# Optimization experiments

Hardware: AMD Instinct MI355X
Metric: run time of the kernel (lower is better)

## Reference

```python
import jax, jax.numpy as jnp
import numpy as np

B, S, HID = 1, 2048, 3072
NH, NKV, HD = 24, 8, 128
ROT = 96
OP = NH * HD + 2 * NKV * HD
MASK_VALUE = -jnp.finfo(jnp.float32).max


def setup_inputs() -> dict:
    key = jax.random.key(0)
    k1, k2, k3, k4, k5 = jax.random.split(key, 5)
    hidden_states = jax.random.normal(k1, (B, S, HID), dtype=jnp.float32)
    # rotary embeddings: use actual cos/sin of rope angles for realism
    inv_freq = 1.0 / (10000.0 ** (jnp.arange(0, ROT, 2, dtype=jnp.float32) / ROT))
    t = jnp.arange(S, dtype=jnp.float32)
    freqs = jnp.outer(t, inv_freq)  # [S, ROT/2]
    emb = jnp.concatenate([freqs, freqs], axis=-1)  # [S, ROT]
    cos = jnp.broadcast_to(jnp.cos(emb)[None], (B, S, ROT))
    sin = jnp.broadcast_to(jnp.sin(emb)[None], (B, S, ROT))
    attention_mask = jnp.ones((B, S), dtype=bool)
    w_qkv = jax.random.normal(k2, (OP, HID), dtype=jnp.float32) * (HID ** -0.5)
    w_o = jax.random.normal(k3, (HID, HID), dtype=jnp.float32) * (HID ** -0.5)
    return {"hidden_states": hidden_states, "cos": cos, "sin": sin,
            "attention_mask": attention_mask, "w_qkv": w_qkv, "w_o": w_o}


def rotate_half(x):
    x1, x2 = jnp.split(x, 2, axis=-1)
    return jnp.concatenate([-x2, x1], axis=-1)


def apply_rope(q, k, cos, sin):
    # cos/sin: [B, S, ROT] -> [B, 1, S, ROT]
    cos = cos[:, None]
    sin = sin[:, None]
    rd = cos.shape[-1]
    q_rot, q_pass = q[..., :rd], q[..., rd:]
    k_rot, k_pass = k[..., :rd], k[..., rd:]
    q = jnp.concatenate([q_rot * cos + rotate_half(q_rot) * sin, q_pass], axis=-1)
    k = jnp.concatenate([k_rot * cos + rotate_half(k_rot) * sin, k_pass], axis=-1)
    return q, k


def reference(hidden_states, cos, sin, attention_mask, w_qkv, w_o):
    b, n, _ = hidden_states.shape
    qkv = hidden_states @ w_qkv.T  # [B, S, OP]
    q, k, v = jnp.split(qkv, [NH * HD, NH * HD + NKV * HD], axis=-1)
    # b n (h d) -> b h n d
    q = q.reshape(b, n, NH, HD).transpose(0, 2, 1, 3)
    k = k.reshape(b, n, NKV, HD).transpose(0, 2, 1, 3)
    v = v.reshape(b, n, NKV, HD).transpose(0, 2, 1, 3)
    q, k = apply_rope(q, k, cos, sin)
    q = q * (HD ** -0.5)
    n_rep = NH // NKV
    if n_rep > 1:
        k = jnp.repeat(k, n_rep, axis=1)
        v = jnp.repeat(v, n_rep, axis=1)
    sim = jnp.einsum('bhid,bhjd->bhij', q, k)
    causal = jnp.triu(jnp.ones((n, n), dtype=bool), k=1)
    sim = jnp.where(causal, MASK_VALUE, sim)
    sim = jnp.where(~attention_mask[:, None, None, :], MASK_VALUE, sim)
    attn = jax.nn.softmax(sim.astype(jnp.float32), axis=-1).astype(v.dtype)
    out = jnp.einsum('bhij,bhjd->bhid', attn, v)
    out = out.transpose(0, 2, 1, 3).reshape(b, n, NH * HD)  # b h n d -> b n (h d)
    return out @ w_o.T
```

## Files before the change

### kernel.cpp

```cpp
#include <hip/hip_runtime.h>

typedef unsigned short u16;
typedef unsigned int u32;
typedef __bf16 bf16x8 __attribute__((ext_vector_type(8)));
typedef float f32x4 __attribute__((ext_vector_type(4)));

#define S_LEN 2048
#define HIDDEN 3072
#define NHEADS 24
#define NKVH 8
#define HDIM 128
#define QKVW 5120
#define QKLD 4096
#define PSTR 80

__device__ __forceinline__ u16 f2bf(float f) {
  u32 u = __float_as_uint(f);
  u32 r = (u + 0x7fffu + ((u >> 16) & 1u)) >> 16;
  return (u16)r;
}
__device__ __forceinline__ float bf2f(u16 h) { return __uint_as_float(((u32)h) << 16); }

__device__ __forceinline__ void gload_lds16(const void* g, void* l) {
  __builtin_amdgcn_global_load_lds((const __attribute__((address_space(1))) void*)g,
                                   (__attribute__((address_space(3))) void*)l, 16, 0, 0);
}

__global__ void cast4(const float4* __restrict__ in, uint2* __restrict__ out, int n4) {
  int i = blockIdx.x * blockDim.x + threadIdx.x;
  if (i >= n4) return;
  float4 f = in[i];
  uint2 o;
  o.x = ((u32)f2bf(f.y) << 16) | f2bf(f.x);
  o.y = ((u32)f2bf(f.w) << 16) | f2bf(f.z);
  out[i] = o;
}

__global__ __launch_bounds__(512, 2) void gemm256(const u16* __restrict__ A,
                                                  const u16* __restrict__ B,
                                                  u16* __restrict__ Cb,
                                                  u16* __restrict__ vtg) {
  __shared__ u16 lds[5][13312];
  const int tid = threadIdx.x;
  const int w = tid >> 6, lane = tid & 63;
  const int wm = w & 3, wn = w >> 2;
  const int l15 = lane & 15, qd = lane >> 4;
  const int K = 3072;
  const int m0 = ((int)blockIdx.x & 7) * 256;
  const int n0 = ((int)blockIdx.x >> 3) * 160;

  size_t offA[2], offB[2];
  int ldsA[2], ldsB[2];
#pragma unroll
  for (int it = 0; it < 2; ++it) {
    int CH = w * 128 + it * 64 + lane;
    int rp = CH >> 3, sl = CH & 7;
    int lin = sl ^ (rp & 7);
    int r = (rp << 1) | (lin >> 2), q = lin & 3;
    offA[it] = (size_t)(m0 + r) * K + q * 8;
    ldsA[it] = (w * 128 + it * 64) * 8;
  }
#pragma unroll
  for (int it = 0; it < 2; ++it) {
    int CH = it * 512 + w * 64 + lane;
    int rp = CH >> 3, sl = CH & 7;
    int lin = sl ^ (rp & 7);
    int r = (rp << 1) | (lin >> 2), q = lin & 3;
    offB[it] = (size_t)(n0 + r) * K + q * 8;
    ldsB[it] = 8192 + (it * 512 + w * 64) * 8;
  }

  int chA[4], chB[5];
#pragma unroll
  for (int i = 0; i < 4; ++i) {
    int r = wm * 64 + i * 16 + l15;
    chA[i] = ((r >> 1) * 8 + ((((r & 1) << 2) | qd) ^ ((r >> 1) & 7))) * 8;
  }
#pragma unroll
  for (int j = 0; j < 5; ++j) {
    int r = wn * 80 + j * 16 + l15;
    chB[j] = 8192 + ((r >> 1) * 8 + ((((r & 1) << 2) | qd) ^ ((r >> 1) & 7))) * 8;
  }

  f32x4 acc[4][5] = {};

  auto stage = [&](int s, int k0) {
    gload_lds16(A + offA[0] + k0, &lds[s][ldsA[0]]);
    gload_lds16(A + offA[1] + k0, &lds[s][ldsA[1]]);
    gload_lds16(B + offB[0] + k0, &lds[s][ldsB[0]]);
    if (w < 2) gload_lds16(B + offB[1] + k0, &lds[s][ldsB[1]]);
  };
  auto rdf = [&](int s, bf16x8 (&Af)[4], bf16x8 (&Bf)[5]) {
#pragma unroll
    for (int i = 0; i < 4; ++i) Af[i] = *(const bf16x8*)&lds[s][chA[i]];
#pragma unroll
    for (int j = 0; j < 5; ++j) Bf[j] = *(const bf16x8*)&lds[s][chB[j]];
  };
  auto mm = [&](bf16x8 (&Af)[4], bf16x8 (&Bf)[5]) {
    __builtin_amdgcn_sched_barrier(0);
    __builtin_amdgcn_s_setprio(1);
#pragma unroll
    for (int i = 0; i < 4; ++i)
#pragma unroll
      for (int j = 0; j < 5; ++j)
        acc[i][j] = __builtin_amdgcn_mfma_f32_16x16x32_bf16(Af[i], Bf[j], acc[i][j], 0, 0, 0);
    __builtin_amdgcn_s_setprio(0);
  };

  stage(0, 0);
  stage(1, 32);
  stage(2, 64);
  stage(3, 96);
  if (w < 2) asm volatile("s_waitcnt vmcnt(8)" ::: "memory");
  else       asm volatile("s_waitcnt vmcnt(6)" ::: "memory");
  __builtin_amdgcn_s_barrier();

  bf16x8 A0[4], B0[5], A1[4], B1[5];
  rdf(0, A0, B0);

  int sp = 4, sc = 1;
  for (int t = 0; t < 92; t += 2) {
    stage(sp, (t + 4) * 32); sp = (sp == 4) ? 0 : sp + 1;
    rdf(sc, A1, B1);         sc = (sc == 4) ? 0 : sc + 1;
    mm(A0, B0);
    if (w < 2) asm volatile("s_waitcnt vmcnt(8)" ::: "memory");
    else       asm volatile("s_waitcnt vmcnt(6)" ::: "memory");
    __builtin_amdgcn_s_barrier();
    stage(sp, (t + 5) * 32); sp = (sp == 4) ? 0 : sp + 1;
    rdf(sc, A0, B0);         sc = (sc == 4) ? 0 : sc + 1;
    mm(A1, B1);
    if (w < 2) asm volatile("s_waitcnt vmcnt(8)" ::: "memory");
    else       asm volatile("s_waitcnt vmcnt(6)" ::: "memory");
    __builtin_amdgcn_s_barrier();
  }
  rdf(3, A1, B1);
  mm(A0, B0);
  if (w < 2) asm volatile("s_waitcnt vmcnt(4)" ::: "memory");
  else       asm volatile("s_waitcnt vmcnt(3)" ::: "memory");
  __builtin_amdgcn_s_barrier();
  rdf(4, A0, B0);
  mm(A1, B1);
  asm volatile("s_waitcnt vmcnt(0)" ::: "memory");
  __builtin_amdgcn_s_barrier();
  rdf(0, A1, B1);
  mm(A0, B0);
  mm(A1, B1);

#pragma unroll
  for (int j = 0; j < 5; ++j) {
    const int nf = n0 + wn * 80 + j * 16;
    if (nf >= 4096) {
#pragma unroll
      for (int i = 0; i < 4; ++i) {
        int nv = nf - 4096 + l15;
        int m = m0 + wm * 64 + i * 16 + qd * 4;
        uint2 p;
        p.x = ((u32)f2bf(acc[i][j][1]) << 16) | f2bf(acc[i][j][0]);
        p.y = ((u32)f2bf(acc[i][j][3]) << 16) | f2bf(acc[i][j][2]);
        *(uint2*)&vtg[(size_t)nv * S_LEN + m] = p;
      }
    } else {
#pragma unroll
      for (int i = 0; i < 4; ++i)
#pragma unroll
        for (int r = 0; r < 4; ++r) {
          int m = m0 + wm * 64 + i * 16 + qd * 4 + r;
          Cb[(size_t)m * QKLD + nf + l15] = f2bf(acc[i][j][r]);
        }
    }
  }
}

__global__ __launch_bounds__(512, 2) void gemm2k(const u16* __restrict__ A,
                                                 const u16* __restrict__ B,
                                                 float* __restrict__ C) {
  __shared__ u16 lds[5][10240];
  const int tid = threadIdx.x;
  const int w = tid >> 6, lane = tid & 63;
  const int wm = w & 1, wn = w >> 1;
  const int l15 = lane & 15, qd = lane >> 4;
  const int K = 3072;
  const int xcd = (int)blockIdx.x & 7, idx = (int)blockIdx.x >> 3;
  const int m0 = ((xcd & 1) * 8 + (idx & 7)) * 128;
  const int n0 = ((xcd >> 1) * 4 + (idx >> 3)) * 192;

  size_t offA, offB[2];
  int ldsAo, ldsB[2];
  {
    int CH = w * 64 + lane;
    int rp = CH >> 3, sl = CH & 7;
    int lin = sl ^ (rp & 7);
    int r = (rp << 1) | (lin >> 2), q = lin & 3;
    offA = (size_t)(m0 + r) * K + q * 8;
    ldsAo = (w * 64) * 8;
  }
#pragma unroll
  for (int it = 0; it < 2; ++it) {
    int CHb = (w < 4) ? (w * 128 + it * 64) : (512 + (w - 4) * 64);
    int CH = CHb + lane;
    int rp = CH >> 3, sl = CH & 7;
    int lin = sl ^ (rp & 7);
    int r = (rp << 1) | (lin >> 2), q = lin & 3;
    offB[it] = (size_t)(n0 + r) * K + q * 8;
    ldsB[it] = 4096 + CHb * 8;
  }

  int chA[4], chB[3];
#pragma unroll
  for (int i = 0; i < 4; ++i) {
    int r = wm * 64 + i * 16 + l15;
    chA[i] = ((r >> 1) * 8 + ((((r & 1) << 2) | qd) ^ ((r >> 1) & 7))) * 8;
  }
#pragma unroll
  for (int j = 0; j < 3; ++j) {
    int r = wn * 48 + j * 16 + l15;
    chB[j] = 4096 + ((r >> 1) * 8 + ((((r & 1) << 2) | qd) ^ ((r >> 1) & 7))) * 8;
  }

  f32x4 acc[4][3] = {};

  auto stage = [&](int s, int k0) {
    gload_lds16(A + offA + k0, &lds[s][ldsAo]);
    gload_lds16(B + offB[0] + k0, &lds[s][ldsB[0]]);
    if (w < 4) gload_lds16(B + offB[1] + k0, &lds[s][ldsB[1]]);
  };
  auto rdf = [&](int s, bf16x8 (&Af)[4], bf16x8 (&Bf)[3]) {
#pragma unroll
    for (int i = 0; i < 4; ++i) Af[i] = *(const bf16x8*)&lds[s][chA[i]];
#pragma unroll
    for (int j = 0; j < 3; ++j) Bf[j] = *(const bf16x8*)&lds[s][chB[j]];
  };
  auto mm = [&](bf16x8 (&Af)[4], bf16x8 (&Bf)[3]) {
    __builtin_amdgcn_sched_barrier(0);
    __builtin_amdgcn_s_setprio(1);
#pragma unroll
    for (int i = 0; i < 4; ++i)
#pragma unroll
      for (int j = 0; j < 3; ++j)
        acc[i][j] = __builtin_amdgcn_mfma_f32_16x16x32_bf16(Af[i], Bf[j], acc[i][j], 0, 0, 0);
    __builtin_amdgcn_s_setprio(0);
  };

  stage(0, 0);
  stage(1, 32);
  stage(2, 64);
  stage(3, 96);
  if (w < 4) asm volatile("s_waitcnt vmcnt(6)" ::: "memory");
  else       asm volatile("s_waitcnt vmcnt(4)" ::: "memory");
  __builtin_amdgcn_s_barrier();

  bf16x8 A0[4], B0[3], A1[4], B1[3];
  rdf(0, A0, B0);

  int sp = 4, sc = 1;
  for (int t = 0; t < 92; t += 2) {
    stage(sp, (t + 4) * 32); sp = (sp == 4) ? 0 : sp + 1;
    rdf(sc, A1, B1);         sc = (sc == 4) ? 0 : sc + 1;
    mm(A0, B0);
    if (w < 4) asm volatile("s_waitcnt vmcnt(6)" ::: "memory");
    else       asm volatile("s_waitcnt vmcnt(4)" ::: "memory");
    __builtin_amdgcn_s_barrier();
    stage(sp, (t + 5) * 32); sp = (sp == 4) ? 0 : sp + 1;
    rdf(sc, A0, B0);         sc = (sc == 4) ? 0 : sc + 1;
    mm(A1, B1);
    if (w < 4) asm volatile("s_waitcnt vmcnt(6)" ::: "memory");
    else       asm volatile("s_waitcnt vmcnt(4)" ::: "memory");
    __builtin_amdgcn_s_barrier();
  }
  rdf(3, A1, B1);
  mm(A0, B0);
  if (w < 4) asm volatile("s_waitcnt vmcnt(3)" ::: "memory");
  else       asm volatile("s_waitcnt vmcnt(2)" ::: "memory");
  __builtin_amdgcn_s_barrier();
  rdf(4, A0, B0);
  mm(A1, B1);
  asm volatile("s_waitcnt vmcnt(0)" ::: "memory");
  __builtin_amdgcn_s_barrier();
  rdf(0, A1, B1);
  mm(A0, B0);
  mm(A1, B1);

#pragma unroll
  for (int i = 0; i < 4; ++i)
#pragma unroll
    for (int j = 0; j < 3; ++j)
#pragma unroll
      for (int r = 0; r < 4; ++r) {
        int m = m0 + wm * 64 + i * 16 + qd * 4 + r;
        int n = n0 + wn * 48 + j * 16 + l15;
        C[(size_t)m * HIDDEN + n] = acc[i][j][r];
      }
}

__global__ __launch_bounds__(128) void rope_kernel(u16* __restrict__ qkv,
                                                   const float* __restrict__ cosb,
                                                   const float* __restrict__ sinb) {
  const int s = blockIdx.x;
  const int hh = blockIdx.y;
  const int d = threadIdx.x;
  const bool isq = hh < NHEADS;
  const size_t base = (size_t)s * QKLD + (isq ? hh * HDIM : HIDDEN + (hh - NHEADS) * HDIM);
  const float scale = 0.08838834764831845f;
  if (d < 48) {
    float x1 = bf2f(qkv[base + d]), x2 = bf2f(qkv[base + d + 48]);
    float c1 = cosb[s * 96 + d], s1 = sinb[s * 96 + d];
    float c2 = cosb[s * 96 + d + 48], s2 = sinb[s * 96 + d + 48];
    float o1 = x1 * c1 - x2 * s1;
    float o2 = x2 * c2 + x1 * s2;
    if (isq) { o1 *= scale; o2 *= scale; }
    qkv[base + d] = f2bf(o1);
    qkv[base + d + 48] = f2bf(o2);
  } else if (d >= 96 && isq) {
    qkv[base + d] = f2bf(bf2f(qkv[base + d]) * scale);
  }
}

__global__ __launch_bounds__(256) void flash_kernel(const u16* __restrict__ qkv,
                                                    const u16* __restrict__ vtg,
                                                    u16* __restrict__ ao) {
  __shared__ u16 Ks[4][64 * 32];
  __shared__ u16 Vt[128 * PSTR];
  __shared__ u16 Ps[64 * PSTR];
  const int bid = blockIdx.x;
  const int g = bid & 255, kk3 = bid >> 8;
  const int rank = (kk3 == 1) ? (kk3 << 8) + (255 - g) : (kk3 << 8) + g;
  const int h = rank % NHEADS;
  const int qi = 31 - rank / NHEADS;
  const int q0 = qi * 64;
  const int hkv = h / 3;
  const int tid = threadIdx.x;
  const int w = tid >> 6, lane = tid & 63;
  const int l15 = lane & 15, qd = lane >> 4;
  const int rS = lane >> 2, cS = (lane & 3) * 8;

  bf16x8 qf[4];
#pragma unroll
  for (int kk = 0; kk < 4; ++kk)
    qf[kk] = *(const bf16x8*)&qkv[(size_t)(q0 + w * 16 + l15) * QKLD + h * HDIM + kk * 32 + qd * 8];

  f32x4 o[8] = {};
  float lrow[4] = {0.f, 0.f, 0.f, 0.f};

  const u16* vb = vtg + (size_t)hkv * HDIM * S_LEN;
  const int vd = tid >> 3;
  const int vkv = (tid & 7) * 8;

  for (int kv0 = 0; kv0 <= q0; kv0 += 64) {
    __syncthreads();
#pragma unroll
    for (int t = 0; t < 4; ++t)
      gload_lds16(qkv + (size_t)(kv0 + t * 16 + rS) * QKLD + HIDDEN + hkv * HDIM + w * 32 + cS,
                  &Ks[w][t * 16 * 32]);
#pragma unroll
    for (int it = 0; it < 4; ++it) {
      int d = it * 32 + vd;
      uint4 vv = *(const uint4*)&vb[(size_t)d * S_LEN + kv0 + vkv];
      *(uint4*)&Vt[d * PSTR + vkv] = vv;
    }
    __syncthreads();

    f32x4 sc[4] = {};
#pragma unroll
    for (int j = 0; j < 4; ++j)
#pragma unroll
      for (int kk = 0; kk < 4; ++kk) {
        bf16x8 kf = *(const bf16x8*)&Ks[kk][(j * 16 + l15) * 32 + qd * 8];
        sc[j] = __builtin_amdgcn_mfma_f32_16x16x32_bf16(qf[kk], kf, sc[j], 0, 0, 0);
      }

    if (kv0 == q0) {
#pragma unroll
      for (int j = 0; j < 4; ++j)
#pragma unroll
        for (int r = 0; r < 4; ++r) {
          int row = w * 16 + qd * 4 + r;
          int col = j * 16 + l15;
          if (col > row) sc[j][r] = -1.0e30f;
        }
    }

#pragma unroll
    for (int j = 0; j < 4; ++j)
#pragma unroll
      for (int r = 0; r < 4; ++r) sc[j][r] = __expf(sc[j][r]);
#pragma unroll
    for (int r = 0; r < 4; ++r)
      lrow[r] += (sc[0][r] + sc[1][r]) + (sc[2][r] + sc[3][r]);

#pragma unroll
    for (int j = 0; j < 4; ++j)
#pragma unroll
      for (int r = 0; r < 4; ++r)
        Ps[(w * 16 + qd * 4 + r) * PSTR + j * 16 + l15] = f2bf(sc[j][r]);
    asm volatile("s_waitcnt lgkmcnt(0)" ::: "memory");

    bf16x8 pf[2];
#pragma unroll
    for (int kk = 0; kk < 2; ++kk)
      pf[kk] = *(const bf16x8*)&Ps[(w * 16 + l15) * PSTR + kk * 32 + qd * 8];
#pragma unroll
    for (int jn = 0; jn < 8; ++jn)
#pragma unroll
      for (int kk = 0; kk < 2; ++kk) {
        bf16x8 vf = *(const bf16x8*)&Vt[(jn * 16 + l15) * PSTR + kk * 32 + qd * 8];
        o[jn] = __builtin_amdgcn_mfma_f32_16x16x32_bf16(pf[kk], vf, o[jn], 0, 0, 0);
      }
  }

  float rinv[4];
#pragma unroll
  for (int r = 0; r < 4; ++r) {
    float s = lrow[r];
#pragma unroll
    for (int d = 1; d < 16; d <<= 1) s += __shfl_xor(s, d, 64);
    rinv[r] = 1.0f / s;
  }
#pragma unroll
  for (int jn = 0; jn < 8; ++jn)
#pragma unroll
    for (int r = 0; r < 4; ++r) {
      int row = q0 + w * 16 + qd * 4 + r;
      ao[(size_t)row * HIDDEN + h * HDIM + jn * 16 + l15] = f2bf(o[jn][r] * rinv[r]);
    }
}

extern "C" void kernel_launch(void* const* d_in, const int* in_sizes, int n_in,
                              void* d_out, int out_size, void* d_ws, size_t ws_size,
                              hipStream_t stream) {
  (void)in_sizes; (void)n_in; (void)out_size; (void)ws_size;
  const float* hs   = (const float*)d_in[0];
  const float* cosb = (const float*)d_in[1];
  const float* sinb = (const float*)d_in[2];
  const float* wqkv = (const float*)d_in[4];
  const float* wo   = (const float*)d_in[5];
  float* out = (float*)d_out;
  char* ws = (char*)d_ws;

  u16* hB   = (u16*)ws;
  u16* wB   = (u16*)(ws + 12582912);
  u16* qkvB = (u16*)(ws + 44040192);
  u16* vtgB = (u16*)(ws + 60817408);
  u16* aoB  = hB;
  u16* woB  = wB;

  cast4<<<6144, 256, 0, stream>>>((const float4*)hs, (uint2*)hB, 1572864);
  cast4<<<15360, 256, 0, stream>>>((const float4*)wqkv, (uint2*)wB, 3932160);
  gemm256<<<256, 512, 0, stream>>>(hB, wB, qkvB, vtgB);
  cast4<<<9216, 256, 0, stream>>>((const float4*)wo, (uint2*)woB, 2359296);
  rope_kernel<<<dim3(2048, 32), 128, 0, stream>>>(qkvB, cosb, sinb);
  flash_kernel<<<768, 256, 0, stream>>>(qkvB, vtgB, aoB);
  gemm2k<<<256, 512, 0, stream>>>(aoB, woB, out);
}
```

Before: 353.1 us.

## Load GEMM A-operand fragments directly from global into registers, stage only B in LDS

The QKV projection GEMM stops staging the A tile through shared memory. Each wave now reads its own A rows straight from global memory into registers, two k-steps ahead, while only the B tile still goes through the 5-stage LDS pipeline. This cuts LDS footprint and LDS read traffic and could allow higher occupancy. The cost is that A loads are no longer shared across the two N-waves, so global/L2 traffic for A doubles. The loads are also uncoalesced 16-byte row reads, and the hand-tuned vmcnt wait counts must exactly match the new load mix.

```diff
diff --git a/kernel.cpp b/kernel.cpp
--- a/kernel.cpp
+++ b/kernel.cpp
@@ -40,7 +40,7 @@
                                                   const u16* __restrict__ B,
                                                   u16* __restrict__ Cb,
                                                   u16* __restrict__ vtg) {
-  __shared__ u16 lds[5][13312];
+  __shared__ u16 lds[5][5120];
   const int tid = threadIdx.x;
   const int w = tid >> 6, lane = tid & 63;
   const int wm = w & 3, wn = w >> 2;
@@ -49,17 +49,8 @@
   const int m0 = ((int)blockIdx.x & 7) * 256;
   const int n0 = ((int)blockIdx.x >> 3) * 160;
 
-  size_t offA[2], offB[2];
-  int ldsA[2], ldsB[2];
-#pragma unroll
-  for (int it = 0; it < 2; ++it) {
-    int CH = w * 128 + it * 64 + lane;
-    int rp = CH >> 3, sl = CH & 7;
-    int lin = sl ^ (rp & 7);
-    int r = (rp << 1) | (lin >> 2), q = lin & 3;
-    offA[it] = (size_t)(m0 + r) * K + q * 8;
-    ldsA[it] = (w * 128 + it * 64) * 8;
-  }
+  size_t offB[2];
+  int ldsB[2];
 #pragma unroll
   for (int it = 0; it < 2; ++it) {
     int CH = it * 512 + w * 64 + lane;
@@ -67,84 +58,82 @@
     int lin = sl ^ (rp & 7);
     int r = (rp << 1) | (lin >> 2), q = lin & 3;
     offB[it] = (size_t)(n0 + r) * K + q * 8;
-    ldsB[it] = 8192 + (it * 512 + w * 64) * 8;
-  }
-
-  int chA[4], chB[5];
-#pragma unroll
-  for (int i = 0; i < 4; ++i) {
-    int r = wm * 64 + i * 16 + l15;
-    chA[i] = ((r >> 1) * 8 + ((((r & 1) << 2) | qd) ^ ((r >> 1) & 7))) * 8;
-  }
+    ldsB[it] = (it * 512 + w * 64) * 8;
+  }
+
+  int chB[5];
 #pragma unroll
   for (int j = 0; j < 5; ++j) {
     int r = wn * 80 + j * 16 + l15;
-    chB[j] = 8192 + ((r >> 1) * 8 + ((((r & 1) << 2) | qd) ^ ((r >> 1) & 7))) * 8;
-  }
+    chB[j] = ((r >> 1) * 8 + ((((r & 1) << 2) | qd) ^ ((r >> 1) & 7))) * 8;
+  }
+
+  const u16* aRow = A + (size_t)(m0 + wm * 64 + l15) * K + qd * 8;
 
   f32x4 acc[4][5] = {};
 
-  auto stage = [&](int s, int k0) {
-    gload_lds16(A + offA[0] + k0, &lds[s][ldsA[0]]);
-    gload_lds16(A + offA[1] + k0, &lds[s][ldsA[1]]);
+  auto stageB = [&](int s, int k0) {
     gload_lds16(B + offB[0] + k0, &lds[s][ldsB[0]]);
     if (w < 2) gload_lds16(B + offB[1] + k0, &lds[s][ldsB[1]]);
   };
-  auto rdf = [&](int s, bf16x8 (&Af)[4], bf16x8 (&Bf)[5]) {
-#pragma unroll
-    for (int i = 0; i < 4; ++i) Af[i] = *(const bf16x8*)&lds[s][chA[i]];
-#pragma unroll
-    for (int j = 0; j < 5; ++j) Bf[j] = *(const bf16x8*)&lds[s][chB[j]];
-  };
-  auto mm = [&](bf16x8 (&Af)[4], bf16x8 (&Bf)[5]) {
-    __builtin_amdgcn_sched_barrier(0);
+  auto loadA = [&](bf16x8 (&Af)[4], int k0) {
+#pragma unroll
+    for (int i = 0; i < 4; ++i)
+      Af[i] = *(const bf16x8*)(aRow + (size_t)i * 16 * K + k0);
+  };
+  auto mm = [&](int s, bf16x8 (&Af)[4]) {
+    bf16x8 b[5];
+#pragma unroll
+    for (int j = 0; j < 5; ++j) b[j] = *(const bf16x8*)&lds[s][chB[j]];
     __builtin_amdgcn_s_setprio(1);
 #pragma unroll
     for (int i = 0; i < 4; ++i)
 #pragma unroll
       for (int j = 0; j < 5; ++j)
-        acc[i][j] = __builtin_amdgcn_mfma_f32_16x16x32_bf16(Af[i], Bf[j], acc[i][j], 0, 0, 0);
+        acc[i][j] = __builtin_amdgcn_mfma_f32_16x16x32_bf16(Af[i], b[j], acc[i][j], 0, 0, 0);
     __builtin_amdgcn_s_setprio(0);
   };
 
-  stage(0, 0);
-  stage(1, 32);
-  stage(2, 64);
-  stage(3, 96);
-  if (w < 2) asm volatile("s_waitcnt vmcnt(8)" ::: "memory");
-  else       asm volatile("s_waitcnt vmcnt(6)" ::: "memory");
-  __builtin_amdgcn_s_barrier();
-
-  bf16x8 A0[4], B0[5], A1[4], B1[5];
-  rdf(0, A0, B0);
-
-  int sp = 4, sc = 1;
+  bf16x8 A0[4], A1[4];
+
+  stageB(0, 0);
+  stageB(1, 32);
+  stageB(2, 64);
+  loadA(A0, 0);
+  loadA(A1, 32);
+  if (w < 2) asm volatile("s_waitcnt vmcnt(4)" ::: "memory");
+  else       asm volatile("s_waitcnt vmcnt(2)" ::: "memory");
+  __builtin_amdgcn_s_barrier();
+
   for (int t = 0; t < 92; t += 2) {
-    stage(sp, (t + 4) * 32); sp = (sp == 4) ? 0 : sp + 1;
-    rdf(sc, A1, B1);         sc = (sc == 4) ? 0 : sc + 1;
-    mm(A0, B0);
-    if (w < 2) asm volatile("s_waitcnt vmcnt(8)" ::: "memory");
-    else       asm volatile("s_waitcnt vmcnt(6)" ::: "memory");
+    stageB((t + 3) % 5, (t + 3) * 32);
+    mm(t % 5, A0);
+    loadA(A0, (t + 2) * 32);
+    if (w < 2) asm volatile("s_waitcnt vmcnt(12)" ::: "memory");
+    else       asm volatile("s_waitcnt vmcnt(10)" ::: "memory");
     __builtin_amdgcn_s_barrier();
-    stage(sp, (t + 5) * 32); sp = (sp == 4) ? 0 : sp + 1;
-    rdf(sc, A0, B0);         sc = (sc == 4) ? 0 : sc + 1;
-    mm(A1, B1);
-    if (w < 2) asm volatile("s_waitcnt vmcnt(8)" ::: "memory");
-    else       asm volatile("s_waitcnt vmcnt(6)" ::: "memory");
+    stageB((t + 4) % 5, (t + 4) * 32);
+    mm((t + 1) % 5, A1);
+    loadA(A1, (t + 3) * 32);
+    if (w < 2) asm volatile("s_waitcnt vmcnt(12)" ::: "memory");
+    else       asm volatile("s_waitcnt vmcnt(10)" ::: "memory");
     __builtin_amdgcn_s_barrier();
   }
-  rdf(3, A1, B1);
-  mm(A0, B0);
-  if (w < 2) asm volatile("s_waitcnt vmcnt(4)" ::: "memory");
-  else       asm volatile("s_waitcnt vmcnt(3)" ::: "memory");
-  __builtin_amdgcn_s_barrier();
-  rdf(4, A0, B0);
-  mm(A1, B1);
-  asm volatile("s_waitcnt vmcnt(0)" ::: "memory");
-  __builtin_amdgcn_s_barrier();
-  rdf(0, A1, B1);
-  mm(A0, B0);
-  mm(A1, B1);
+  stageB(0, 95 * 32);
+  mm(2, A0);
+  loadA(A0, 94 * 32);
+  if (w < 2) asm volatile("s_waitcnt vmcnt(12)" ::: "memory");
+  else       asm volatile("s_waitcnt vmcnt(10)" ::: "memory");
+  __builtin_amdgcn_s_barrier();
+  mm(3, A1);
+  loadA(A1, 95 * 32);
+  if (w < 2) asm volatile("s_waitcnt vmcnt(10)" ::: "memory");
+  else       asm volatile("s_waitcnt vmcnt(9)" ::: "memory");
+  __builtin_amdgcn_s_barrier();
+  mm(4, A0);
+  asm volatile("s_waitcnt vmcnt(4)" ::: "memory");
+  __builtin_amdgcn_s_barrier();
+  mm(0, A1);
 
 #pragma unroll
   for (int j = 0; j < 5; ++j) {
```

New measurement: 410.4 us. 16.2% more time.
